# Optimization experiments

Hardware: AMD Instinct MI355X
Metric: run time of the kernel (lower is better)

## Reference

```python
import jax, jax.numpy as jnp
import numpy as np


def setup_inputs() -> dict:
    key = jax.random.key(0)
    k1, k2, k3 = jax.random.split(key, 3)
    B, C, P = 16384, 2048, 256
    f_struct = jax.random.normal(k1, (B, C), dtype=jnp.float32)
    pids = jax.random.randint(k2, (B,), 0, P, dtype=jnp.int64)
    camids = jax.random.randint(k3, (B,), 0, 2, dtype=jnp.int64)
    return {"f_struct": f_struct, "pids": pids, "camids": camids, "num_pids": P}


def reference(f_struct, pids, camids, num_pids):
    # Fused segment reduction over joint (pid, camid) groups: seg = pid*2 + camid
    seg = (pids * 2 + camids).astype(jnp.int32)
    n_seg = num_pids * 2
    sums = jax.ops.segment_sum(f_struct, seg, num_segments=n_seg)          # [2P, C]
    counts = jax.ops.segment_sum(jnp.ones_like(seg, dtype=f_struct.dtype),
                                 seg, num_segments=n_seg)                   # [2P]
    means = sums / jnp.maximum(counts, 1)[:, None]                          # safe mean
    means = means.reshape(num_pids, 2, -1)                                  # [P, 2, C]
    counts = counts.reshape(num_pids, 2)                                    # [P, 2]
    # per-pid MSE between visible (cam 0) and thermal (cam 1) centers
    diff = means[:, 0, :] - means[:, 1, :]
    mse = jnp.mean(diff * diff, axis=-1)                                    # [P]
    valid = (counts[:, 0] > 0) & (counts[:, 1] > 0)                         # [P]
    cnt = jnp.sum(valid.astype(f_struct.dtype))
    loss = jnp.sum(jnp.where(valid, mse, 0.0)) / jnp.maximum(cnt, 1)
    return jnp.where(cnt > 0, loss, jnp.zeros((), dtype=f_struct.dtype))
```

## Files before the change

kernel.cpp:

```cpp
#include <hip/hip_runtime.h>

#define NPID   256
#define CCOLS  2048
#define NCHUNK 2
#define CHUNKW 1024
#define CAP    1024


__device__ __forceinline__ void gather_cam(const float* __restrict__ base,
                                           const int* __restrict__ list,
                                           int cnt, float4& acc)
{
    int n8 = cnt & ~7;
    if (n8 > 0) {
        float4 v[8];
#pragma unroll
        for (int k = 0; k < 8; ++k)
            v[k] = *reinterpret_cast<const float4*>(base + (size_t)list[k] * CCOLS);
        for (int i = 8; i < n8; i += 8) {
            float4 w[8];
#pragma unroll
            for (int k = 0; k < 8; ++k)
                w[k] = *reinterpret_cast<const float4*>(base + (size_t)list[i + k] * CCOLS);
#pragma unroll
            for (int k = 0; k < 8; ++k) {
                acc.x += v[k].x; acc.y += v[k].y; acc.z += v[k].z; acc.w += v[k].w;
                v[k] = w[k];
            }
        }
#pragma unroll
        for (int k = 0; k < 8; ++k) {
            acc.x += v[k].x; acc.y += v[k].y; acc.z += v[k].z; acc.w += v[k].w;
        }
    }
    for (int i = n8; i < cnt; ++i) {
        float4 vv = *reinterpret_cast<const float4*>(base + (size_t)list[i] * CCOLS);
        acc.x += vv.x; acc.y += vv.y; acc.z += vv.z; acc.w += vv.w;
    }
}

__global__ __launch_bounds__(256) void gather_k(
    const float* __restrict__ f, const int* __restrict__ pids,
    const int* __restrict__ camids, float* __restrict__ part,
    float* __restrict__ vflag, int B)
{
    __shared__ int list0[CAP], list1[CAP];
    __shared__ int cur0, cur1;

    int p     = blockIdx.x >> 1;
    int chunk = blockIdx.x & 1;
    int t     = threadIdx.x;

    if (t == 0) { cur0 = 0; cur1 = 0; }
    __syncthreads();

    for (int i = t; i < B; i += 256) {
        if (pids[i] == p) {
            if (camids[i] == 0) {
                int pos = atomicAdd(&cur0, 1);
                if (pos < CAP) list0[pos] = i;
            } else {
                int pos = atomicAdd(&cur1, 1);
                if (pos < CAP) list1[pos] = i;
            }
        }
    }
    __syncthreads();
    int c0 = min(cur0, CAP), c1 = min(cur1, CAP);

    const float* base = f + (size_t)chunk * CHUNKW + (size_t)t * 4;
    float4 acc0 = make_float4(0.f, 0.f, 0.f, 0.f);
    float4 acc1 = make_float4(0.f, 0.f, 0.f, 0.f);
    gather_cam(base, list0, c0, acc0);
    gather_cam(base, list1, c1, acc1);

    float i0 = 1.0f / (float)(c0 > 0 ? c0 : 1);
    float i1 = 1.0f / (float)(c1 > 0 ? c1 : 1);
    float dx = acc0.x * i0 - acc1.x * i1;
    float dy = acc0.y * i0 - acc1.y * i1;
    float dz = acc0.z * i0 - acc1.z * i1;
    float dw = acc0.w * i0 - acc1.w * i1;
    float sq = dx * dx + dy * dy + dz * dz + dw * dw;

    for (int off = 32; off; off >>= 1) sq += __shfl_down(sq, off);
    __shared__ float wred[4];
    if ((t & 63) == 0) wred[t >> 6] = sq;
    __syncthreads();
    if (t == 0) {
        part[blockIdx.x] = wred[0] + wred[1] + wred[2] + wred[3];
        if (chunk == 0) vflag[p] = (c0 > 0 && c1 > 0) ? 1.0f : 0.0f;
    }
}

__global__ __launch_bounds__(256) void reduce_k(
    const float* __restrict__ part, const float* __restrict__ vflag,
    float* __restrict__ out)
{
    int t = threadIdx.x;
    float mse   = (part[2 * t] + part[2 * t + 1]) * (1.0f / (float)CCOLS);
    float valid = vflag[t];
    float num   = valid * mse;
    float cv    = valid;
    for (int off = 32; off; off >>= 1) {
        num += __shfl_down(num, off);
        cv  += __shfl_down(cv, off);
    }
    __shared__ float nred[4], cred[4];
    if ((t & 63) == 0) { nred[t >> 6] = num; cred[t >> 6] = cv; }
    __syncthreads();
    if (t == 0) {
        float N  = nred[0] + nred[1] + nred[2] + nred[3];
        float Cv = cred[0] + cred[1] + cred[2] + cred[3];
        out[0] = (Cv > 0.0f) ? (N / fmaxf(Cv, 1.0f)) : 0.0f;
    }
}

extern "C" void kernel_launch(void* const* d_in, const int* in_sizes, int n_in,
                              void* d_out, int out_size, void* d_ws, size_t ws_size,
                              hipStream_t stream)
{
    const float* f      = (const float*)d_in[0];
    const int*   pids   = (const int*)d_in[1];
    const int*   camids = (const int*)d_in[2];

    int B = in_sizes[1];

    float* part  = (float*)d_ws;
    float* vflag = (float*)((char*)d_ws + 2048);

    gather_k<<<NPID * NCHUNK, 256, 0, stream>>>(f, pids, camids, part, vflag, B);
    reduce_k<<<1, 256, 0, stream>>>(part, vflag, (float*)d_out);
}
```

Baseline: 223.7 us.

## Replace per-pid gather with column-tiled LDS scatter-add segment reduction

Drops the per-pid gather kernel, where every block rescanned all B labels and then read rows at random. In its place, each block owns a 64-column tile and a slab of rows, streams those rows in order, and scatter-adds them into a shared-memory table of 512 segments. Per-slab partial sums are written out, or combined with global atomics when workspace is small, and a second kernel finishes the per-pid means and MSE. This removes the redundant label scans and the uncoalesced row gathers. In exchange it adds LDS atomic contention, a 128KB shared table that limits occupancy, and extra partial-sum traffic of about 32MB in the non-atomic path.

```diff
diff --git a/kernel.cpp b/kernel.cpp
--- a/kernel.cpp
+++ b/kernel.cpp
@@ -1,106 +1,140 @@
 #include <hip/hip_runtime.h>
 
+#define BB     16384
+#define CC     2048
+#define NSEG   512
 #define NPID   256
-#define CCOLS  2048
-#define NCHUNK 2
-#define CHUNKW 1024
-#define CAP    1024
+#define WTILE  64
+#define NTILE  (CC / WTILE)
+#define NSLAB  8
+#define SLABR  (BB / NSLAB)
+#define TPB    1024
+#define RPW    (SLABR / (TPB/64))
 
+template <bool ATOMIC>
+__global__ __launch_bounds__(TPB) void stage1_k(
+    const float* __restrict__ f, const int* __restrict__ pids,
+    const int* __restrict__ camids,
+    float* __restrict__ part,
+    float* __restrict__ cnt_part)
+{
+    __shared__ float table[NSEG * WTILE];
+    __shared__ int   seg_s[SLABR];
+    __shared__ float cnt_s[NSEG];
 
-__device__ __forceinline__ void gather_cam(const float* __restrict__ base,
-                                           const int* __restrict__ list,
-                                           int cnt, float4& acc)
-{
-    int n8 = cnt & ~7;
-    if (n8 > 0) {
-        float4 v[8];
+    const int tile = blockIdx.x;
+    const int slab = blockIdx.y;
+    const int t    = threadIdx.x;
+    const int r0   = slab * SLABR;
+
+    for (int i = t; i < NSEG * WTILE; i += TPB) table[i] = 0.0f;
+    for (int i = t; i < NSEG; i += TPB) cnt_s[i] = 0.0f;
+    for (int j = t; j < SLABR; j += TPB)
+        seg_s[j] = pids[r0 + j] * 2 + camids[r0 + j];
+    __syncthreads();
+
+    const int wv = t >> 6, ln = t & 63;
+    const int jbase = wv * RPW;
+    const float* fp = f + (size_t)(r0 + jbase) * CC + tile * WTILE + ln;
+    const bool docnt = (tile == 0) && (ln == 0);
+
+    for (int j = 0; j < RPW; j += 8) {
+        float v[8]; int sg[8];
 #pragma unroll
-        for (int k = 0; k < 8; ++k)
-            v[k] = *reinterpret_cast<const float4*>(base + (size_t)list[k] * CCOLS);
-        for (int i = 8; i < n8; i += 8) {
-            float4 w[8];
+        for (int k = 0; k < 8; ++k) v[k] = fp[(size_t)(j + k) * CC];
 #pragma unroll
-            for (int k = 0; k < 8; ++k)
-                w[k] = *reinterpret_cast<const float4*>(base + (size_t)list[i + k] * CCOLS);
-#pragma unroll
-            for (int k = 0; k < 8; ++k) {
-                acc.x += v[k].x; acc.y += v[k].y; acc.z += v[k].z; acc.w += v[k].w;
-                v[k] = w[k];
-            }
-        }
+        for (int k = 0; k < 8; ++k) sg[k] = seg_s[jbase + j + k];
 #pragma unroll
         for (int k = 0; k < 8; ++k) {
-            acc.x += v[k].x; acc.y += v[k].y; acc.z += v[k].z; acc.w += v[k].w;
+            atomicAdd(&table[sg[k] * WTILE + ln], v[k]);
+            if (docnt) atomicAdd(&cnt_s[sg[k]], 1.0f);
         }
     }
-    for (int i = n8; i < cnt; ++i) {
-        float4 vv = *reinterpret_cast<const float4*>(base + (size_t)list[i] * CCOLS);
-        acc.x += vv.x; acc.y += vv.y; acc.z += vv.z; acc.w += vv.w;
+    __syncthreads();
+
+    if (ATOMIC) {
+        for (int i = t; i < NSEG * WTILE; i += TPB) {
+            int sg = i >> 6, c = i & 63;
+            atomicAdd(&part[(size_t)sg * CC + tile * WTILE + c], table[i]);
+        }
+        if (tile == 0)
+            for (int i = t; i < NSEG; i += TPB) atomicAdd(&cnt_part[i], cnt_s[i]);
+    } else {
+        for (int i = t; i < NSEG * WTILE; i += TPB) {
+            int sg = i >> 6, c = i & 63;
+            part[((size_t)slab * NSEG + sg) * CC + tile * WTILE + c] = table[i];
+        }
+        if (tile == 0)
+            for (int i = t; i < NSEG; i += TPB) cnt_part[slab * NSEG + i] = cnt_s[i];
     }
 }
 
-__global__ __launch_bounds__(256) void gather_k(
-    const float* __restrict__ f, const int* __restrict__ pids,
-    const int* __restrict__ camids, float* __restrict__ part,
-    float* __restrict__ vflag, int B)
+template <bool ATOMIC>
+__global__ __launch_bounds__(TPB) void stage2_k(
+    const float* __restrict__ part, const float* __restrict__ cnt_part,
+    float* __restrict__ mse, float* __restrict__ valid)
 {
-    __shared__ int list0[CAP], list1[CAP];
-    __shared__ int cur0, cur1;
+    const int p = blockIdx.x;
+    const int t = threadIdx.x;
 
-    int p     = blockIdx.x >> 1;
-    int chunk = blockIdx.x & 1;
-    int t     = threadIdx.x;
-
-    if (t == 0) { cur0 = 0; cur1 = 0; }
-    __syncthreads();
-
-    for (int i = t; i < B; i += 256) {
-        if (pids[i] == p) {
-            if (camids[i] == 0) {
-                int pos = atomicAdd(&cur0, 1);
-                if (pos < CAP) list0[pos] = i;
-            } else {
-                int pos = atomicAdd(&cur1, 1);
-                if (pos < CAP) list1[pos] = i;
+    __shared__ float c0s, c1s;
+    if (t == 0) {
+        float c0 = 0.f, c1 = 0.f;
+        if (ATOMIC) { c0 = cnt_part[2 * p]; c1 = cnt_part[2 * p + 1]; }
+        else {
+#pragma unroll
+            for (int s = 0; s < NSLAB; ++s) {
+                c0 += cnt_part[s * NSEG + 2 * p];
+                c1 += cnt_part[s * NSEG + 2 * p + 1];
             }
         }
+        c0s = c0; c1s = c1;
     }
     __syncthreads();
-    int c0 = min(cur0, CAP), c1 = min(cur1, CAP);
+    const float c0 = c0s, c1 = c1s;
+    const float i0 = 1.0f / fmaxf(c0, 1.0f);
+    const float i1 = 1.0f / fmaxf(c1, 1.0f);
 
-    const float* base = f + (size_t)chunk * CHUNKW + (size_t)t * 4;
-    float4 acc0 = make_float4(0.f, 0.f, 0.f, 0.f);
-    float4 acc1 = make_float4(0.f, 0.f, 0.f, 0.f);
-    gather_cam(base, list0, c0, acc0);
-    gather_cam(base, list1, c1, acc1);
+    float acc = 0.0f;
+#pragma unroll
+    for (int q = 0; q < CC / TPB; ++q) {
+        const int col = t + q * TPB;
+        float s0 = 0.f, s1 = 0.f;
+        if (ATOMIC) {
+            s0 = part[(size_t)(2 * p) * CC + col];
+            s1 = part[(size_t)(2 * p + 1) * CC + col];
+        } else {
+#pragma unroll
+            for (int s = 0; s < NSLAB; ++s) {
+                s0 += part[((size_t)s * NSEG + 2 * p) * CC + col];
+                s1 += part[((size_t)s * NSEG + 2 * p + 1) * CC + col];
+            }
+        }
+        float d = s0 * i0 - s1 * i1;
+        acc += d * d;
+    }
 
-    float i0 = 1.0f / (float)(c0 > 0 ? c0 : 1);
-    float i1 = 1.0f / (float)(c1 > 0 ? c1 : 1);
-    float dx = acc0.x * i0 - acc1.x * i1;
-    float dy = acc0.y * i0 - acc1.y * i1;
-    float dz = acc0.z * i0 - acc1.z * i1;
-    float dw = acc0.w * i0 - acc1.w * i1;
-    float sq = dx * dx + dy * dy + dz * dz + dw * dw;
-
-    for (int off = 32; off; off >>= 1) sq += __shfl_down(sq, off);
-    __shared__ float wred[4];
-    if ((t & 63) == 0) wred[t >> 6] = sq;
+    for (int off = 32; off; off >>= 1) acc += __shfl_down(acc, off);
+    __shared__ float wred[TPB / 64];
+    if ((t & 63) == 0) wred[t >> 6] = acc;
     __syncthreads();
     if (t == 0) {
-        part[blockIdx.x] = wred[0] + wred[1] + wred[2] + wred[3];
-        if (chunk == 0) vflag[p] = (c0 > 0 && c1 > 0) ? 1.0f : 0.0f;
+        float tot = 0.f;
+#pragma unroll
+        for (int w = 0; w < TPB / 64; ++w) tot += wred[w];
+        mse[p]   = tot * (1.0f / (float)CC);
+        valid[p] = (c0 > 0.f && c1 > 0.f) ? 1.0f : 0.0f;
     }
 }
 
 __global__ __launch_bounds__(256) void reduce_k(
-    const float* __restrict__ part, const float* __restrict__ vflag,
+    const float* __restrict__ mse, const float* __restrict__ valid,
     float* __restrict__ out)
 {
     int t = threadIdx.x;
-    float mse   = (part[2 * t] + part[2 * t + 1]) * (1.0f / (float)CCOLS);
-    float valid = vflag[t];
-    float num   = valid * mse;
-    float cv    = valid;
+    float v   = valid[t];
+    float num = v * mse[t];
+    float cv  = v;
     for (int off = 32; off; off >>= 1) {
         num += __shfl_down(num, off);
         cv  += __shfl_down(cv, off);
@@ -123,11 +157,31 @@
     const int*   pids   = (const int*)d_in[1];
     const int*   camids = (const int*)d_in[2];
 
-    int B = in_sizes[1];
+    const size_t PART_BYTES = (size_t)NSLAB * NSEG * CC * 4;
+    const size_t CNTP_BYTES = (size_t)NSLAB * NSEG * 4;
+    const size_t SUMS_BYTES = (size_t)NSEG * CC * 4;
+    const size_t CNTA_BYTES = (size_t)NSEG * 4;
 
-    float* part  = (float*)d_ws;
-    float* vflag = (float*)((char*)d_ws + 2048);
+    dim3 g1(NTILE, NSLAB);
 
-    gather_k<<<NPID * NCHUNK, 256, 0, stream>>>(f, pids, camids, part, vflag, B);
-    reduce_k<<<1, 256, 0, stream>>>(part, vflag, (float*)d_out);
+    if (ws_size >= PART_BYTES + CNTP_BYTES + 4096) {
+        float* part  = (float*)d_ws;
+        float* cntp  = (float*)((char*)d_ws + PART_BYTES);
+        float* mse   = (float*)((char*)d_ws + PART_BYTES + CNTP_BYTES);
+        float* valid = (float*)((char*)d_ws + PART_BYTES + CNTP_BYTES + 1024);
+
+        stage1_k<false><<<g1, TPB, 0, stream>>>(f, pids, camids, part, cntp);
+        stage2_k<false><<<NPID, TPB, 0, stream>>>(part, cntp, mse, valid);
+        reduce_k<<<1, 256, 0, stream>>>(mse, valid, (float*)d_out);
+    } else {
+        float* sums  = (float*)d_ws;
+        float* cnta  = (float*)((char*)d_ws + SUMS_BYTES);
+        float* mse   = (float*)((char*)d_ws + SUMS_BYTES + CNTA_BYTES);
+        float* valid = (float*)((char*)d_ws + SUMS_BYTES + CNTA_BYTES + 1024);
+
+        hipMemsetAsync(d_ws, 0, SUMS_BYTES + CNTA_BYTES, stream);
+        stage1_k<true><<<g1, TPB, 0, stream>>>(f, pids, camids, sums, cnta);
+        stage2_k<true><<<NPID, TPB, 0, stream>>>(sums, cnta, mse, valid);
+        reduce_k<<<1, 256, 0, stream>>>(mse, valid, (float*)d_out);
+    }
 }
```

After: 327.9 us. 46.6% more time.
